# Performance work log

Hardware: AMD Instinct MI355X
Metric: run time of the kernel (lower is better)

## Reference

```python
import math
import jax, jax.numpy as jnp
import numpy as np

SCALE = 64.0
MARGIN = 0.5
COS_M = math.cos(MARGIN)
SIN_M = math.sin(MARGIN)
TH = math.cos(math.pi - MARGIN)
MM = math.sin(math.pi - MARGIN) * MARGIN
EPS = 1e-12  # F.normalize default eps

B, D, C = 2048, 512, 100000


def setup_inputs() -> dict:
    key = jax.random.key(0)
    k1, k2, k3 = jax.random.split(key, 3)
    embeddings = jax.random.normal(k1, (B, D), dtype=jnp.float32)
    labels = jax.random.randint(k2, (B,), 0, C, dtype=jnp.int64)
    # xavier-uniform-like init for weight [C, D]
    limit = math.sqrt(6.0 / (C + D))
    weight = jax.random.uniform(k3, (C, D), dtype=jnp.float32, minval=-limit, maxval=limit)
    return {"embeddings": embeddings, "labels": labels, "weight": weight}


def _l2norm(x):
    n = jnp.linalg.norm(x, axis=-1, keepdims=True)
    return x / jnp.maximum(n, EPS)


def reference(embeddings, labels, weight):
    cosine = _l2norm(embeddings) @ _l2norm(weight).T  # [B, C]
    sine = jnp.sqrt(jnp.clip(1.0 - cosine * cosine, 0.0, None))
    phi = cosine * COS_M - sine * SIN_M
    phi = jnp.where(cosine > TH, phi, cosine - MM)
    # one-hot blend without materializing a separate one-hot tensor
    col = jnp.arange(cosine.shape[1])[None, :]
    is_target = col == labels[:, None]  # [B, C] bool
    logits = jnp.where(is_target, phi, cosine)
    return logits * SCALE
```

## Files before the change

### kernel.cpp

```cpp
#include <hip/hip_runtime.h>
#include <hip/hip_bf16.h>
#include <math.h>

constexpr int Bq = 2048;
constexpr int Dq = 512;
constexpr int Cq = 100000;
constexpr int NPAD = 100096;

constexpr float SCALE = 64.0f;
constexpr float COS_M = 0.8775825618903728f;
constexpr float SIN_M = 0.479425538604203f;
constexpr float THR   = -0.8775825618903728f;
constexpr float MM    = 0.2397127693021015f;

typedef __attribute__((ext_vector_type(8))) __bf16 bf16x8;
typedef __attribute__((ext_vector_type(4))) float f32x4;

typedef const __attribute__((address_space(1))) unsigned int guint;
typedef __attribute__((address_space(3))) unsigned int suint;

__device__ __forceinline__ void gload_lds16(const unsigned short* g, unsigned short* lds)
{
    __builtin_amdgcn_global_load_lds((guint*)g, (suint*)lds, 16, 0, 0);
}

__device__ __forceinline__ unsigned int pack_bf16x2(float lo, float hi)
{
    __hip_bfloat16 h0 = __float2bfloat16(lo);
    __hip_bfloat16 h1 = __float2bfloat16(hi);
    return ((unsigned int)(*(unsigned short*)&h1) << 16) |
           (unsigned int)(*(unsigned short*)&h0);
}

__global__ __launch_bounds__(256) void normalize_rows_kernel(
    const float* __restrict__ in, unsigned short* __restrict__ out, int nrows)
{
    const int w = threadIdx.x >> 6, lane = threadIdx.x & 63;
    const int row = blockIdx.x * 4 + w;
    float4 a = {0.f, 0.f, 0.f, 0.f}, b = a;
    if (row < nrows) {
        const float4* src = reinterpret_cast<const float4*>(in + (size_t)row * Dq);
        a = src[lane];
        b = src[lane + 64];
    }
    float ss = a.x * a.x + a.y * a.y + a.z * a.z + a.w * a.w
             + b.x * b.x + b.y * b.y + b.z * b.z + b.w * b.w;
    #pragma unroll
    for (int off = 32; off > 0; off >>= 1) ss += __shfl_down(ss, off);
    ss = __shfl(ss, 0);
    const float invn = 1.0f / fmaxf(sqrtf(ss), 1e-12f);

    uint2* out64 = reinterpret_cast<uint2*>(out + (size_t)row * Dq);
    uint2 pa, pb;
    pa.x = pack_bf16x2(a.x * invn, a.y * invn);
    pa.y = pack_bf16x2(a.z * invn, a.w * invn);
    pb.x = pack_bf16x2(b.x * invn, b.y * invn);
    pb.y = pack_bf16x2(b.z * invn, b.w * invn);
    out64[lane] = pa;
    out64[lane + 64] = pb;
}

__global__ __launch_bounds__(512, 1) void arc_gemm_kernel(
    const unsigned short* __restrict__ A,
    const unsigned short* __restrict__ Bn,
    const int* __restrict__ labels,
    float* __restrict__ out)
{
    extern __shared__ unsigned short lds[];

    const int cpx = (int)gridDim.x >> 3;
    const int bid = ((int)blockIdx.x & 7) * cpx + ((int)blockIdx.x >> 3);
    const int tm = bid & 7;
    const int tn = bid >> 3;
    const int m0 = tm * 256, n0 = tn * 256;

    const int t = threadIdx.x;
    const int w = t >> 6, lane = t & 63;
    const int wr = (w >> 2) * 128;
    const int wc = (w & 3) * 64;
    const int fr = lane & 15, kg = lane >> 4;
    const int s7 = fr & 7;
    const int c0 = (kg ^ s7) * 8;
    const int c1 = ((4 + kg) ^ s7) * 8;

    const int trow = t >> 3;
    const int tch = ((t & 7) ^ (trow & 7)) * 8;
    const unsigned short* gA = A  + (size_t)(m0 + trow) * Dq + tch;
    const unsigned short* gB = Bn + (size_t)(n0 + trow) * Dq + tch;
    const int dstA = trow * 64 + (t & 7) * 8;

#define STAGE_A(buf, u, kts) gload_lds16(gA + (size_t)(u) * 64 * Dq + (size_t)(kts) * 64, \
                                         &lds[(buf) * 32768 + (u) * 4096 + dstA])
#define STAGE_B(buf, u, kts) gload_lds16(gB + (size_t)(u) * 64 * Dq + (size_t)(kts) * 64, \
                                         &lds[(buf) * 32768 + 16384 + (u) * 4096 + dstA])
#define BARRIER() do { __builtin_amdgcn_sched_barrier(0); __builtin_amdgcn_s_barrier(); } while (0)

    f32x4 acc[8][4];
    #pragma unroll
    for (int i = 0; i < 8; ++i)
        #pragma unroll
        for (int j = 0; j < 4; ++j) acc[i][j] = {0.f, 0.f, 0.f, 0.f};

    STAGE_A(0, 0, 0); STAGE_A(0, 1, 0); STAGE_A(0, 2, 0); STAGE_A(0, 3, 0);
    STAGE_B(0, 0, 0); STAGE_B(0, 1, 0); STAGE_B(0, 2, 0); STAGE_B(0, 3, 0);
    STAGE_B(1, 0, 1); STAGE_B(1, 1, 1); STAGE_B(1, 2, 1); STAGE_B(1, 3, 1);
    STAGE_A(1, 0, 1); STAGE_A(1, 2, 1);
    asm volatile("s_waitcnt vmcnt(6)" ::: "memory");
    __builtin_amdgcn_s_barrier();

    const int arow = (wr + fr) * 64;
    const int brow = 16384 + (wc + fr) * 64;

#define LDA(q) do { \
    _Pragma("unroll") for (int m2 = 0; m2 < 2; ++m2) { \
        afr[m2][0] = *reinterpret_cast<const bf16x8*>(&lds[cbo + arow + ((q) * 32 + m2 * 16) * 64 + c0]); \
        afr[m2][1] = *reinterpret_cast<const bf16x8*>(&lds[cbo + arow + ((q) * 32 + m2 * 16) * 64 + c1]); } \
} while (0)
#define LDB() do { \
    _Pragma("unroll") for (int ni = 0; ni < 4; ++ni) { \
        bfr[ni][0] = *reinterpret_cast<const bf16x8*>(&lds[cbo + brow + ni * 1024 + c0]); \
        bfr[ni][1] = *reinterpret_cast<const bf16x8*>(&lds[cbo + brow + ni * 1024 + c1]); } \
} while (0)
#define MFMA_QUAD(q) do { \
    __builtin_amdgcn_s_setprio(1); \
    _Pragma("unroll") for (int ks = 0; ks < 2; ++ks) \
    _Pragma("unroll") for (int m2 = 0; m2 < 2; ++m2) \
    _Pragma("unroll") for (int ni = 0; ni < 4; ++ni) \
        acc[2 * (q) + m2][ni] = __builtin_amdgcn_mfma_f32_16x16x32_bf16( \
            bfr[ni][ks], afr[m2][ks], acc[2 * (q) + m2][ni], 0, 0, 0); \
    __builtin_amdgcn_s_setprio(0); \
} while (0)

    #pragma unroll
    for (int kt = 0; kt < 8; ++kt) {
        const int cb = kt & 1, nb = cb ^ 1;
        const int cbo = cb * 32768;
        bf16x8 bfr[4][2];
        {
            bf16x8 afr[2][2];
            LDB(); LDA(0);
            if (kt < 7) { STAGE_A(nb, 1, kt + 1); STAGE_A(nb, 3, kt + 1); }
            BARRIER();
            MFMA_QUAD(0);
            BARRIER();
            LDA(1);
            if (kt < 6) { STAGE_B(cb, 0, kt + 2); STAGE_B(cb, 1, kt + 2); }
            BARRIER();
            MFMA_QUAD(1);
            BARRIER();
            LDA(2);
            if (kt < 6) { STAGE_B(cb, 2, kt + 2); STAGE_B(cb, 3, kt + 2); }
            BARRIER();
            MFMA_QUAD(2);
            BARRIER();
            LDA(3);
            if (kt < 6) { STAGE_A(cb, 0, kt + 2); STAGE_A(cb, 2, kt + 2); }
            BARRIER();
            MFMA_QUAD(3);
            if (kt < 6) asm volatile("s_waitcnt vmcnt(6)" ::: "memory");
            else        asm volatile("s_waitcnt vmcnt(0)" ::: "memory");
            BARRIER();
        }
    }

    const int ccol0 = wc + kg * 4;
    #pragma unroll
    for (int mi = 0; mi < 8; ++mi) {
        const int grow = m0 + wr + mi * 16 + fr;
        const int lab = labels[grow];
        float* orow = out + (size_t)grow * Cq + n0;
        #pragma unroll
        for (int ni = 0; ni < 4; ++ni) {
            const int col0 = ccol0 + ni * 16;
            const int gcol0 = n0 + col0;
            if (gcol0 >= Cq) continue;
            f32x4 v = acc[mi][ni];
            #pragma unroll
            for (int r = 0; r < 4; ++r) {
                if (gcol0 + r == lab) {
                    float c = v[r];
                    float sine = sqrtf(fmaxf(1.0f - c * c, 0.0f));
                    float phi = c * COS_M - sine * SIN_M;
                    v[r] = (c > THR) ? phi : (c - MM);
                }
            }
            v *= SCALE;
            __builtin_nontemporal_store(v, reinterpret_cast<f32x4*>(orow + col0));
        }
    }
#undef STAGE_A
#undef STAGE_B
#undef BARRIER
#undef LDA
#undef LDB
#undef MFMA_QUAD
}

extern "C" void kernel_launch(void* const* d_in, const int* in_sizes, int n_in,
                              void* d_out, int out_size, void* d_ws, size_t ws_size,
                              hipStream_t stream)
{
    const float* emb    = (const float*)d_in[0];
    const int*   labels = (const int*)d_in[1];
    const float* weight = (const float*)d_in[2];
    float* out = (float*)d_out;

    unsigned short* Abf = (unsigned short*)d_ws;
    unsigned short* Bbf = Abf + (size_t)Bq * Dq;

    normalize_rows_kernel<<<Bq / 4, 256, 0, stream>>>(emb, Abf, Bq);
    normalize_rows_kernel<<<NPAD / 4, 256, 0, stream>>>(weight, Bbf, Cq);
    arc_gemm_kernel<<<8 * (NPAD / 256), 512, 131072, stream>>>(Abf, Bbf, labels, out);
}
```

Baseline: 382.9 us.

## Stage GEMM epilogue through LDS for coalesced full-row output stores

The epilogue now writes the scaled accumulator tiles into shared memory in 64-row chunks. All 512 threads then read them back and issue contiguous 1 KB row segments of nontemporal stores to the 800 MB output. Before, each lane stored scattered 16-byte fragments across rows, which hurt write coalescing on this store-bound kernel. The cost is extra LDS traffic and eight block-wide barriers per tile, where half the warps sit idle during each staging phase.

Result: faster. 371.4 us (-3.0%).

```diff
diff --git a/kernel.cpp b/kernel.cpp
--- a/kernel.cpp
+++ b/kernel.cpp
@@ -163,30 +163,47 @@
         }
     }
 
-    const int ccol0 = wc + kg * 4;
-    #pragma unroll
-    for (int mi = 0; mi < 8; ++mi) {
-        const int grow = m0 + wr + mi * 16 + fr;
-        const int lab = labels[grow];
-        float* orow = out + (size_t)grow * Cq + n0;
-        #pragma unroll
-        for (int ni = 0; ni < 4; ++ni) {
-            const int col0 = ccol0 + ni * 16;
-            const int gcol0 = n0 + col0;
-            if (gcol0 >= Cq) continue;
-            f32x4 v = acc[mi][ni];
+    float* lf = reinterpret_cast<float*>(lds);
+    #pragma unroll
+    for (int p = 0; p < 4; ++p) {
+        if ((w >> 2) == (p >> 1)) {
             #pragma unroll
-            for (int r = 0; r < 4; ++r) {
-                if (gcol0 + r == lab) {
-                    float c = v[r];
-                    float sine = sqrtf(fmaxf(1.0f - c * c, 0.0f));
-                    float phi = c * COS_M - sine * SIN_M;
-                    v[r] = (c > THR) ? phi : (c - MM);
+            for (int j = 0; j < 4; ++j) {
+                const int mi = (p & 1) * 4 + j;
+                const int lrow = j * 16 + fr;
+                const int lab = labels[m0 + p * 64 + lrow];
+                #pragma unroll
+                for (int ni = 0; ni < 4; ++ni) {
+                    const int col0 = wc + ni * 16 + kg * 4;
+                    const int gcol0 = n0 + col0;
+                    f32x4 v = acc[mi][ni];
+                    #pragma unroll
+                    for (int r = 0; r < 4; ++r) {
+                        if (gcol0 + r == lab) {
+                            float c = v[r];
+                            float sine = sqrtf(fmaxf(1.0f - c * c, 0.0f));
+                            float phi = c * COS_M - sine * SIN_M;
+                            v[r] = (c > THR) ? phi : (c - MM);
+                        }
+                    }
+                    v *= SCALE;
+                    *reinterpret_cast<f32x4*>(&lf[lrow * 260 + col0]) = v;
                 }
             }
-            v *= SCALE;
-            __builtin_nontemporal_store(v, reinterpret_cast<f32x4*>(orow + col0));
         }
+        __syncthreads();
+        const int cc = t & 63, rh = t >> 6;
+        #pragma unroll
+        for (int s = 0; s < 8; ++s) {
+            const int lrow = s * 8 + rh;
+            f32x4 v = *reinterpret_cast<const f32x4*>(&lf[lrow * 260 + cc * 4]);
+            const int gcol0 = n0 + cc * 4;
+            if (gcol0 < Cq)
+                __builtin_nontemporal_store(
+                    v, reinterpret_cast<f32x4*>(
+                        out + (size_t)(m0 + p * 64 + lrow) * Cq + gcol0));
+        }
+        __syncthreads();
     }
 #undef STAGE_A
 #undef STAGE_B
```
